# Kernel optimization log

Measured on AMD Instinct MI355X. Metric: run time of the kernel, lower is better.

Reference implementation:

```python
import jax, jax.numpy as jnp
import numpy as np

N, E, C = 25000, 400000, 64
NUM_ELEM, NUM_BESSEL, HID, NPATH, L = 4, 8, 64, 5, 2
R_MAX, AVG_NN = 5.0, 16.0
SQRT3, SQRT2 = 3.0 ** 0.5, 2.0 ** 0.5


def setup_inputs() -> dict:
    key = jax.random.key(0)
    ks = jax.random.split(key, 16)
    def w(k, shape, fan_in):
        return jax.random.normal(k, shape, jnp.float32) / np.float32(np.sqrt(fan_in))
    return {
        "positions": jax.random.normal(ks[0], (N, 3), jnp.float32),
        "species": jax.random.randint(ks[1], (N,), 0, NUM_ELEM, jnp.int32),
        "edge_index": jax.random.randint(ks[2], (2, E), 0, N, jnp.int32),
        "node_embed_W": w(ks[3], (NUM_ELEM, C), NUM_ELEM),
        "lin_up_W0": w(ks[4], (L, C, C), C),
        "lin_up_W1": w(ks[5], (L, C, C), C),
        "mlp_W1": w(ks[6], (L, NUM_BESSEL, HID), NUM_BESSEL),
        "mlp_W2": w(ks[7], (L, HID, HID), HID),
        "mlp_W3": w(ks[8], (L, HID, NPATH * C), HID),
        "lin_W0": w(ks[9], (L, C, C), C),
        "lin_W1": w(ks[10], (L, C, C), C),
        "prod_W0": w(ks[11], (L, NUM_ELEM, 3, C), 3),
        "prod_W1": w(ks[12], (L, NUM_ELEM, 2, C), 2),
        "prod_lin_W0": w(ks[13], (L, C, C), C),
        "prod_lin_W1": w(ks[14], (L, C, C), C),
    }


def _poly_cutoff(r):  # MACE polynomial cutoff, p=6
    p = 6.0
    x = r / R_MAX
    f = (1.0 - 0.5 * (p + 1.0) * (p + 2.0) * x ** 6
         + p * (p + 2.0) * x ** 7 - 0.5 * p * (p + 1.0) * x ** 8)
    return f * (x < 1.0)


def reference(positions, species, edge_index, node_embed_W,
              lin_up_W0, lin_up_W1, mlp_W1, mlp_W2, mlp_W3,
              lin_W0, lin_W1, prod_W0, prod_W1, prod_lin_W0, prod_lin_W1):
    sender, receiver = edge_index[0], edge_index[1]
    vec = positions[sender] - positions[receiver]                  # [E,3]
    r = jnp.maximum(jnp.linalg.norm(vec, axis=-1), 1e-6)           # [E]
    u = vec / r[:, None]
    Y1 = SQRT3 * u                                                 # l=1 SH (component norm); Y0 == 1
    # Bessel radial embedding with polynomial cutoff -> edge_feats [E, NUM_BESSEL]
    n = jnp.arange(1, NUM_BESSEL + 1, dtype=jnp.float32)
    bessel = jnp.sqrt(2.0 / R_MAX) * jnp.sin(n[None, :] * jnp.pi * r[:, None] / R_MAX) / r[:, None]
    edge_feats = bessel * _poly_cutoff(r)[:, None]
    node_attrs = jax.nn.one_hot(species, NUM_ELEM, dtype=jnp.float32)  # [N,4]
    h0 = node_attrs @ node_embed_W                                 # [N,C] scalars
    h1 = jnp.zeros((N, C, 3), jnp.float32)                         # [N,C,3] vectors
    for l in range(L):
        # linear up-projection (per-l channel mixing)
        x0 = h0 @ lin_up_W0[l]
        x1 = jnp.einsum('ncd,ck->nkd', h1, lin_up_W1[l])
        # per-edge radial MLP -> tensor-product path weights [E,5,C]
        tpw = jax.nn.silu(edge_feats @ mlp_W1[l])
        tpw = jax.nn.silu(tpw @ mlp_W2[l])
        tpw = (tpw @ mlp_W3[l]).reshape(E, NPATH, C)
        xs0, xs1 = x0[sender], x1[sender]                          # gather senders
        # CG tensor product (uvu): paths 0x0->0, 0x1->1, 1x0->1, 1x1->0, 1x1->1
        m0 = tpw[:, 0] * xs0 + tpw[:, 3] * (jnp.einsum('ecd,ed->ec', xs1, Y1) / SQRT3)
        m1 = (tpw[:, 1][..., None] * xs0[..., None] * Y1[:, None, :]
              + tpw[:, 2][..., None] * xs1
              + tpw[:, 4][..., None] * jnp.cross(xs1, Y1[:, None, :]) / SQRT2)
        # scatter-sum aggregation over receivers
        M0 = jax.ops.segment_sum(m0, receiver, num_segments=N) / AVG_NN
        M1 = jax.ops.segment_sum(m1, receiver, num_segments=N) / AVG_NN
        h0 = M0 @ lin_W0[l]
        h1 = jnp.einsum('ncd,ck->nkd', M1, lin_W1[l])
        # equivariant product basis (correlation-2 symmetric contraction, element-dependent weights)
        pw0 = jnp.einsum('ne,epc->npc', node_attrs, prod_W0[l])    # [N,3,C]
        paths0 = jnp.stack([h0, h0 * h0, (h1 * h1).sum(-1) / SQRT3], axis=1)
        b0 = (pw0 * paths0).sum(1)
        pw1 = jnp.einsum('ne,epc->npc', node_attrs, prod_W1[l])    # [N,2,C]
        b1 = pw1[:, 0][..., None] * h1 + pw1[:, 1][..., None] * (h0[..., None] * h1)
        h0 = b0 @ prod_lin_W0[l]
        h1 = jnp.einsum('ncd,ck->nkd', b1, prod_lin_W1[l])
    return jnp.concatenate([h0[..., None], h1], axis=-1)           # [N,C,4]
```

## Files before the change

kernel.cpp:

```cpp
#include <hip/hip_runtime.h>
#include <math.h>

#define CDIM 64
#define NBES 8

#define SQRT3_F     1.7320508075688772f
#define INV_SQRT3_F 0.57735026918962576f
#define INV_SQRT2_F 0.70710678118654752f
#define INV_AVG_NN  0.0625f

__device__ __forceinline__ float silu(float x) {
    return x / (1.0f + expf(-x));
}

__global__ __launch_bounds__(256) void k_lin0(
    float* __restrict__ h0, float* __restrict__ h1,
    const int* __restrict__ species, const float* __restrict__ embedW,
    const float* __restrict__ W0, float* __restrict__ x0, int nnodes) {
    const int w = threadIdx.x >> 6, k = threadIdx.x & 63;
    const int n = blockIdx.x * 4 + w;
    if (n >= nnodes) return;
    const float* er = embedW + species[n] * 64;
    float a0 = 0.f;
    for (int c = 0; c < 64; ++c) a0 = fmaf(er[c], W0[c * 64 + k], a0);
    x0[n * 64 + k] = a0;
    h0[n * 64 + k] = 0.f;
    h1[n * 192 + k] = 0.f;
    h1[n * 192 + 64 + k] = 0.f;
    h1[n * 192 + 128 + k] = 0.f;
}

__global__ __launch_bounds__(320, 4) void k_edge0(
    const float* __restrict__ pos, const int* __restrict__ eidx,
    const float* __restrict__ x0,
    const float* __restrict__ W1, const float* __restrict__ W2,
    const float* __restrict__ W3,
    float* __restrict__ M0, float* __restrict__ M1, int nedges) {
    __shared__ __align__(16) float sFEAT[64][8];
    __shared__ float sY1[64][3];
    __shared__ int sSend[64];
    __shared__ int sRecv[64];
    __shared__ __align__(16) float sH2[64 * 68];
    __shared__ __align__(16) float sU0[4352];

    float* const sH1T = sU0;
    float* const sTP = sU0;

    const int t = threadIdx.x;
    const int wv = t >> 6;

    if (t < 64) {
        int e = blockIdx.x * 64 + t;
        int s = 0, r = 0;
        float y0 = 0.f, y1 = 0.f, y2 = 0.f;
        float feats[NBES];
#pragma unroll
        for (int b = 0; b < NBES; ++b) feats[b] = 0.f;
        if (e < nedges) {
            s = eidx[e];
            r = eidx[nedges + e];
            double dx = (double)pos[3 * s + 0] - (double)pos[3 * r + 0];
            double dy = (double)pos[3 * s + 1] - (double)pos[3 * r + 1];
            double dz = (double)pos[3 * s + 2] - (double)pos[3 * r + 2];
            double rr = sqrt(dx * dx + dy * dy + dz * dz);
            if (rr < 1e-6) rr = 1e-6;
            double inv = 1.0 / rr;
            y0 = (float)(1.7320508075688772 * dx * inv);
            y1 = (float)(1.7320508075688772 * dy * inv);
            y2 = (float)(1.7320508075688772 * dz * inv);
            double xx = rr * 0.2;
            double f = 0.0;
            if (xx < 1.0) {
                double x2 = xx * xx, x3 = x2 * xx, x6 = x3 * x3;
                f = 1.0 - 28.0 * x6 + 48.0 * x6 * xx - 21.0 * x6 * x2;
            }
            double pref = 0.63245553203367587 * f * inv;
#pragma unroll
            for (int b = 0; b < NBES; ++b) {
                double arg = (double)(b + 1) * 3.14159265358979324 * rr * 0.2;
                feats[b] = (float)(sin(arg) * pref);
            }
        }
        sSend[t] = s;
        sRecv[t] = r;
        sY1[t][0] = y0; sY1[t][1] = y1; sY1[t][2] = y2;
#pragma unroll
        for (int b = 0; b < NBES; ++b) sFEAT[t][b] = feats[b];
    }
    __syncthreads();

    if (t < 256) {
        const int j = t & 63;
        float w1c[NBES];
#pragma unroll
        for (int b = 0; b < NBES; ++b) w1c[b] = W1[b * 64 + j];
#pragma unroll
        for (int i = 0; i < 16; ++i) {
            int el = wv * 16 + i;
            const float4* fr = (const float4*)(&sFEAT[el][0]);
            float4 f0 = fr[0], f1 = fr[1];
            float acc = 0.f;
            acc = fmaf(f0.x, w1c[0], acc);
            acc = fmaf(f0.y, w1c[1], acc);
            acc = fmaf(f0.z, w1c[2], acc);
            acc = fmaf(f0.w, w1c[3], acc);
            acc = fmaf(f1.x, w1c[4], acc);
            acc = fmaf(f1.y, w1c[5], acc);
            acc = fmaf(f1.z, w1c[6], acc);
            acc = fmaf(f1.w, w1c[7], acc);
            sH1T[j * 68 + el] = silu(acc);
        }
    }
    __syncthreads();

    if (t < 256) {
        const int eg = t >> 4;
        const int j4 = (t & 15) * 4;
        float a00 = 0.f, a01 = 0.f, a02 = 0.f, a03 = 0.f;
        float a10 = 0.f, a11 = 0.f, a12 = 0.f, a13 = 0.f;
        float a20 = 0.f, a21 = 0.f, a22 = 0.f, a23 = 0.f;
        float a30 = 0.f, a31 = 0.f, a32 = 0.f, a33 = 0.f;
#pragma unroll 4
        for (int k = 0; k < 64; ++k) {
            float4 av = *(const float4*)&sH1T[k * 68 + 4 * eg];
            float4 wv4 = *(const float4*)&W2[k * 64 + j4];
            a00 = fmaf(av.x, wv4.x, a00); a01 = fmaf(av.x, wv4.y, a01);
            a02 = fmaf(av.x, wv4.z, a02); a03 = fmaf(av.x, wv4.w, a03);
            a10 = fmaf(av.y, wv4.x, a10); a11 = fmaf(av.y, wv4.y, a11);
            a12 = fmaf(av.y, wv4.z, a12); a13 = fmaf(av.y, wv4.w, a13);
            a20 = fmaf(av.z, wv4.x, a20); a21 = fmaf(av.z, wv4.y, a21);
            a22 = fmaf(av.z, wv4.z, a22); a23 = fmaf(av.z, wv4.w, a23);
            a30 = fmaf(av.w, wv4.x, a30); a31 = fmaf(av.w, wv4.y, a31);
            a32 = fmaf(av.w, wv4.z, a32); a33 = fmaf(av.w, wv4.w, a33);
        }
        *(float4*)&sH2[(4 * eg + 0) * 68 + j4] =
            make_float4(silu(a00), silu(a01), silu(a02), silu(a03));
        *(float4*)&sH2[(4 * eg + 1) * 68 + j4] =
            make_float4(silu(a10), silu(a11), silu(a12), silu(a13));
        *(float4*)&sH2[(4 * eg + 2) * 68 + j4] =
            make_float4(silu(a20), silu(a21), silu(a22), silu(a23));
        *(float4*)&sH2[(4 * eg + 3) * 68 + j4] =
            make_float4(silu(a30), silu(a31), silu(a32), silu(a33));
    }
    __syncthreads();

    const int eb16 = t & 15;
    const int cb8 = (t >> 4) * 8;
    float acc[4][8];
#pragma unroll
    for (int i = 0; i < 4; ++i)
#pragma unroll
        for (int j = 0; j < 8; ++j) acc[i][j] = 0.f;

    if (t < 256) {
#pragma unroll 1
        for (int kt = 0; kt < 16; ++kt) {
            float4 h[4];
#pragma unroll
            for (int i = 0; i < 4; ++i)
                h[i] = *(const float4*)&sH2[(i * 16 + eb16) * 68 + kt * 4];
#pragma unroll
            for (int kk = 0; kk < 4; ++kk) {
                const int k = kt * 4 + kk;
                float4 wa = *(const float4*)&W3[k * 320 + cb8];
                float4 wb = *(const float4*)&W3[k * 320 + cb8 + 4];
#pragma unroll
                for (int i = 0; i < 4; ++i) {
                    float hv = (kk == 0) ? h[i].x
                             : (kk == 1) ? h[i].y
                             : (kk == 2) ? h[i].z
                                         : h[i].w;
                    acc[i][0] = fmaf(hv, wa.x, acc[i][0]);
                    acc[i][1] = fmaf(hv, wa.y, acc[i][1]);
                    acc[i][2] = fmaf(hv, wa.z, acc[i][2]);
                    acc[i][3] = fmaf(hv, wa.w, acc[i][3]);
                    acc[i][4] = fmaf(hv, wb.x, acc[i][4]);
                    acc[i][5] = fmaf(hv, wb.y, acc[i][5]);
                    acc[i][6] = fmaf(hv, wb.z, acc[i][6]);
                    acc[i][7] = fmaf(hv, wb.w, acc[i][7]);
                }
            }
        }
    }

    const int p0 = cb8 >> 6;
    const int c0 = cb8 & 63;
#pragma unroll
    for (int g = 0; g < 4; ++g) {
        if (t < 256) {
            const int row = (p0 * 16 + eb16) * 68 + c0;
            *(float4*)&sTP[row] =
                make_float4(acc[g][0], acc[g][1], acc[g][2], acc[g][3]);
            *(float4*)&sTP[row + 4] =
                make_float4(acc[g][4], acc[g][5], acc[g][6], acc[g][7]);
        }
        __syncthreads();
        for (int v = t; v < 1024; v += 320) {
            int i = v >> 6, cc = v & 63;
            int el = g * 16 + i;
            int s = sSend[el], r = sRecv[el];
            float X0 = x0[s * 64 + cc];
            float Yx = sY1[el][0], Yy = sY1[el][1], Yz = sY1[el][2];
            float t0 = sTP[(0 * 16 + i) * 68 + cc];
            float t1 = sTP[(1 * 16 + i) * 68 + cc];
            float m0 = t0 * X0;
            float m1 = t1 * X0 * INV_AVG_NN;
            atomicAdd(&M0[r * 64 + cc], m0 * INV_AVG_NN);
            atomicAdd(&M1[r * 192 + cc], m1 * Yx);
            atomicAdd(&M1[r * 192 + 64 + cc], m1 * Yy);
            atomicAdd(&M1[r * 192 + 128 + cc], m1 * Yz);
        }
        __syncthreads();
    }
}

__global__ __launch_bounds__(320, 4) void k_edge(
    const float* __restrict__ pos, const int* __restrict__ eidx,
    const float* __restrict__ x0, const float* __restrict__ x1,
    const float* __restrict__ W1, const float* __restrict__ W2,
    const float* __restrict__ W3,
    float* __restrict__ M0, float* __restrict__ M1, int nedges) {
    __shared__ __align__(16) float sFEAT[64][8];
    __shared__ float sY1[64][3];
    __shared__ int sSend[64];
    __shared__ int sRecv[64];
    __shared__ __align__(16) float sH2[64 * 68];
    __shared__ __align__(16) float sU[5440];

    float* const sH1T = sU;
    float* const sTP = sU;

    const int t = threadIdx.x;
    const int eb = t & 7;
    const int cb8 = (t >> 3) * 8;
    const int wv = t >> 6;
    const int c0 = cb8 & 63;

    if (t < 64) {
        int e = blockIdx.x * 64 + t;
        int s = 0, r = 0;
        float y0 = 0.f, y1 = 0.f, y2 = 0.f;
        float feats[NBES];
#pragma unroll
        for (int b = 0; b < NBES; ++b) feats[b] = 0.f;
        if (e < nedges) {
            s = eidx[e];
            r = eidx[nedges + e];
            double dx = (double)pos[3 * s + 0] - (double)pos[3 * r + 0];
            double dy = (double)pos[3 * s + 1] - (double)pos[3 * r + 1];
            double dz = (double)pos[3 * s + 2] - (double)pos[3 * r + 2];
            double rr = sqrt(dx * dx + dy * dy + dz * dz);
            if (rr < 1e-6) rr = 1e-6;
            double inv = 1.0 / rr;
            y0 = (float)(1.7320508075688772 * dx * inv);
            y1 = (float)(1.7320508075688772 * dy * inv);
            y2 = (float)(1.7320508075688772 * dz * inv);
            double xx = rr * 0.2;
            double f = 0.0;
            if (xx < 1.0) {
                double x2 = xx * xx, x3 = x2 * xx, x6 = x3 * x3;
                f = 1.0 - 28.0 * x6 + 48.0 * x6 * xx - 21.0 * x6 * x2;
            }
            double pref = 0.63245553203367587 * f * inv;
#pragma unroll
            for (int b = 0; b < NBES; ++b) {
                double arg = (double)(b + 1) * 3.14159265358979324 * rr * 0.2;
                feats[b] = (float)(sin(arg) * pref);
            }
        }
        sSend[t] = s;
        sRecv[t] = r;
        sY1[t][0] = y0; sY1[t][1] = y1; sY1[t][2] = y2;
#pragma unroll
        for (int b = 0; b < NBES; ++b) sFEAT[t][b] = feats[b];
    }
    __syncthreads();

    if (t < 256) {
        const int j = t & 63;
        float w1c[NBES];
#pragma unroll
        for (int b = 0; b < NBES; ++b) w1c[b] = W1[b * 64 + j];
#pragma unroll
        for (int i = 0; i < 16; ++i) {
            int el = wv * 16 + i;
            const float4* fr = (const float4*)(&sFEAT[el][0]);
            float4 f0 = fr[0], f1 = fr[1];
            float acc = 0.f;
            acc = fmaf(f0.x, w1c[0], acc);
            acc = fmaf(f0.y, w1c[1], acc);
            acc = fmaf(f0.z, w1c[2], acc);
            acc = fmaf(f0.w, w1c[3], acc);
            acc = fmaf(f1.x, w1c[4], acc);
            acc = fmaf(f1.y, w1c[5], acc);
            acc = fmaf(f1.z, w1c[6], acc);
            acc = fmaf(f1.w, w1c[7], acc);
            sH1T[j * 68 + el] = silu(acc);
        }
    }
    __syncthreads();

    if (t < 256) {
        const int eg = t >> 4;
        const int j4 = (t & 15) * 4;
        float a00 = 0.f, a01 = 0.f, a02 = 0.f, a03 = 0.f;
        float a10 = 0.f, a11 = 0.f, a12 = 0.f, a13 = 0.f;
        float a20 = 0.f, a21 = 0.f, a22 = 0.f, a23 = 0.f;
        float a30 = 0.f, a31 = 0.f, a32 = 0.f, a33 = 0.f;
#pragma unroll 4
        for (int k = 0; k < 64; ++k) {
            float4 av = *(const float4*)&sH1T[k * 68 + 4 * eg];
            float4 wv4 = *(const float4*)&W2[k * 64 + j4];
            a00 = fmaf(av.x, wv4.x, a00); a01 = fmaf(av.x, wv4.y, a01);
            a02 = fmaf(av.x, wv4.z, a02); a03 = fmaf(av.x, wv4.w, a03);
            a10 = fmaf(av.y, wv4.x, a10); a11 = fmaf(av.y, wv4.y, a11);
            a12 = fmaf(av.y, wv4.z, a12); a13 = fmaf(av.y, wv4.w, a13);
            a20 = fmaf(av.z, wv4.x, a20); a21 = fmaf(av.z, wv4.y, a21);
            a22 = fmaf(av.z, wv4.z, a22); a23 = fmaf(av.z, wv4.w, a23);
            a30 = fmaf(av.w, wv4.x, a30); a31 = fmaf(av.w, wv4.y, a31);
            a32 = fmaf(av.w, wv4.z, a32); a33 = fmaf(av.w, wv4.w, a33);
        }
        *(float4*)&sH2[(4 * eg + 0) * 68 + j4] =
            make_float4(silu(a00), silu(a01), silu(a02), silu(a03));
        *(float4*)&sH2[(4 * eg + 1) * 68 + j4] =
            make_float4(silu(a10), silu(a11), silu(a12), silu(a13));
        *(float4*)&sH2[(4 * eg + 2) * 68 + j4] =
            make_float4(silu(a20), silu(a21), silu(a22), silu(a23));
        *(float4*)&sH2[(4 * eg + 3) * 68 + j4] =
            make_float4(silu(a30), silu(a31), silu(a32), silu(a33));
    }
    __syncthreads();

    float acc[8][8];
#pragma unroll
    for (int i = 0; i < 8; ++i)
#pragma unroll
        for (int j = 0; j < 8; ++j) acc[i][j] = 0.f;

#pragma unroll 1
    for (int kt = 0; kt < 16; ++kt) {
        float4 h[8];
#pragma unroll
        for (int i = 0; i < 8; ++i)
            h[i] = *(const float4*)&sH2[(i * 8 + eb) * 68 + kt * 4];
#pragma unroll
        for (int kk = 0; kk < 4; ++kk) {
            const int k = kt * 4 + kk;
            float4 wa = *(const float4*)&W3[k * 320 + cb8];
            float4 wb = *(const float4*)&W3[k * 320 + cb8 + 4];
#pragma unroll
            for (int i = 0; i < 8; ++i) {
                float hv = (kk == 0) ? h[i].x
                         : (kk == 1) ? h[i].y
                         : (kk == 2) ? h[i].z
                                     : h[i].w;
                acc[i][0] = fmaf(hv, wa.x, acc[i][0]);
                acc[i][1] = fmaf(hv, wa.y, acc[i][1]);
                acc[i][2] = fmaf(hv, wa.z, acc[i][2]);
                acc[i][3] = fmaf(hv, wa.w, acc[i][3]);
                acc[i][4] = fmaf(hv, wb.x, acc[i][4]);
                acc[i][5] = fmaf(hv, wb.y, acc[i][5]);
                acc[i][6] = fmaf(hv, wb.z, acc[i][6]);
                acc[i][7] = fmaf(hv, wb.w, acc[i][7]);
            }
        }
    }

#pragma unroll
    for (int g = 0; g < 4; ++g) {
        {
            const int rowA = (wv * 16 + eb) * 68 + c0;
            const int rowB = (wv * 16 + 8 + eb) * 68 + c0;
            *(float4*)&sTP[rowA] =
                make_float4(acc[2 * g][0], acc[2 * g][1], acc[2 * g][2], acc[2 * g][3]);
            *(float4*)&sTP[rowA + 4] =
                make_float4(acc[2 * g][4], acc[2 * g][5], acc[2 * g][6], acc[2 * g][7]);
            *(float4*)&sTP[rowB] =
                make_float4(acc[2 * g + 1][0], acc[2 * g + 1][1], acc[2 * g + 1][2], acc[2 * g + 1][3]);
            *(float4*)&sTP[rowB + 4] =
                make_float4(acc[2 * g + 1][4], acc[2 * g + 1][5], acc[2 * g + 1][6], acc[2 * g + 1][7]);
        }
        __syncthreads();
        for (int v = t; v < 1024; v += 320) {
            int i = v >> 6, cc = v & 63;
            int el = g * 16 + i;
            int s = sSend[el], r = sRecv[el];
            float X0 = x0[s * 64 + cc];
            float Xx = x1[s * 192 + cc];
            float Xy = x1[s * 192 + 64 + cc];
            float Xz = x1[s * 192 + 128 + cc];
            float Yx = sY1[el][0], Yy = sY1[el][1], Yz = sY1[el][2];
            float t0 = sTP[(0 * 16 + i) * 68 + cc];
            float t1 = sTP[(1 * 16 + i) * 68 + cc];
            float t2 = sTP[(2 * 16 + i) * 68 + cc];
            float t3 = sTP[(3 * 16 + i) * 68 + cc];
            float t4 = sTP[(4 * 16 + i) * 68 + cc];
            float dotp = Xx * Yx + Xy * Yy + Xz * Yz;
            float m0 = t0 * X0 + t3 * (dotp * INV_SQRT3_F);
            float cx = Xy * Yz - Xz * Yy;
            float cy = Xz * Yx - Xx * Yz;
            float cz = Xx * Yy - Xy * Yx;
            float m1x = t1 * X0 * Yx + t2 * Xx + t4 * (cx * INV_SQRT2_F);
            float m1y = t1 * X0 * Yy + t2 * Xy + t4 * (cy * INV_SQRT2_F);
            float m1z = t1 * X0 * Yz + t2 * Xz + t4 * (cz * INV_SQRT2_F);
            atomicAdd(&M0[r * 64 + cc], m0 * INV_AVG_NN);
            atomicAdd(&M1[r * 192 + cc], m1x * INV_AVG_NN);
            atomicAdd(&M1[r * 192 + 64 + cc], m1y * INV_AVG_NN);
            atomicAdd(&M1[r * 192 + 128 + cc], m1z * INV_AVG_NN);
        }
        __syncthreads();
    }
}

__global__ __launch_bounds__(256) void k_nodelin(
    float* __restrict__ h0, float* __restrict__ h1,
    const int* __restrict__ species,
    const float* __restrict__ linW0, const float* __restrict__ linW1,
    const float* __restrict__ prodW0, const float* __restrict__ prodW1,
    const float* __restrict__ plinW0, const float* __restrict__ plinW1,
    const float* __restrict__ lupW0, const float* __restrict__ lupW1,
    float* __restrict__ x0, float* __restrict__ x1, int nnodes) {
    __shared__ float sh[4][4][64];
    const int w = threadIdx.x >> 6, k = threadIdx.x & 63;
    const int n = blockIdx.x * 4 + w;
    const bool valid = n < nnodes;
    float v0 = valid ? h0[n * 64 + k] : 0.f;
    float v1 = valid ? h1[n * 192 + k] : 0.f;
    float v2 = valid ? h1[n * 192 + 64 + k] : 0.f;
    float v3 = valid ? h1[n * 192 + 128 + k] : 0.f;
    sh[w][0][k] = v0; sh[w][1][k] = v1; sh[w][2][k] = v2; sh[w][3][k] = v3;
    if (valid) {
        h0[n * 64 + k] = 0.f;
        h1[n * 192 + k] = 0.f;
        h1[n * 192 + 64 + k] = 0.f;
        h1[n * 192 + 128 + k] = 0.f;
    }
    __syncthreads();
    float a0 = 0.f, a1 = 0.f, a2 = 0.f, a3 = 0.f;
    for (int c = 0; c < 64; ++c) {
        float w0 = linW0[c * 64 + k], w1 = linW1[c * 64 + k];
        a0 = fmaf(sh[w][0][c], w0, a0);
        a1 = fmaf(sh[w][1][c], w1, a1);
        a2 = fmaf(sh[w][2][c], w1, a2);
        a3 = fmaf(sh[w][3][c], w1, a3);
    }
    int sp = valid ? species[n] : 0;
    float p00 = prodW0[sp * 192 + k];
    float p01 = prodW0[sp * 192 + 64 + k];
    float p02 = prodW0[sp * 192 + 128 + k];
    float p10 = prodW1[sp * 128 + k];
    float p11 = prodW1[sp * 128 + 64 + k];
    float nsq = a1 * a1 + a2 * a2 + a3 * a3;
    float b0 = p00 * a0 + p01 * (a0 * a0) + p02 * (nsq * INV_SQRT3_F);
    float b1x = p10 * a1 + p11 * (a0 * a1);
    float b1y = p10 * a2 + p11 * (a0 * a2);
    float b1z = p10 * a3 + p11 * (a0 * a3);
    __syncthreads();
    sh[w][0][k] = b0; sh[w][1][k] = b1x; sh[w][2][k] = b1y; sh[w][3][k] = b1z;
    __syncthreads();
    a0 = a1 = a2 = a3 = 0.f;
    for (int c = 0; c < 64; ++c) {
        float w0 = plinW0[c * 64 + k], w1 = plinW1[c * 64 + k];
        a0 = fmaf(sh[w][0][c], w0, a0);
        a1 = fmaf(sh[w][1][c], w1, a1);
        a2 = fmaf(sh[w][2][c], w1, a2);
        a3 = fmaf(sh[w][3][c], w1, a3);
    }
    __syncthreads();
    sh[w][0][k] = a0; sh[w][1][k] = a1; sh[w][2][k] = a2; sh[w][3][k] = a3;
    __syncthreads();
    a0 = a1 = a2 = a3 = 0.f;
    for (int c = 0; c < 64; ++c) {
        float w0 = lupW0[c * 64 + k], w1 = lupW1[c * 64 + k];
        a0 = fmaf(sh[w][0][c], w0, a0);
        a1 = fmaf(sh[w][1][c], w1, a1);
        a2 = fmaf(sh[w][2][c], w1, a2);
        a3 = fmaf(sh[w][3][c], w1, a3);
    }
    if (valid) {
        x0[n * 64 + k] = a0;
        x1[n * 192 + k] = a1;
        x1[n * 192 + 64 + k] = a2;
        x1[n * 192 + 128 + k] = a3;
    }
}

__global__ __launch_bounds__(256) void k_nodeout(
    const float* __restrict__ h0, const float* __restrict__ h1,
    const int* __restrict__ species,
    const float* __restrict__ linW0, const float* __restrict__ linW1,
    const float* __restrict__ prodW0, const float* __restrict__ prodW1,
    const float* __restrict__ plinW0, const float* __restrict__ plinW1,
    float4* __restrict__ out, int nnodes) {
    __shared__ float sh[4][4][64];
    const int w = threadIdx.x >> 6, k = threadIdx.x & 63;
    const int n = blockIdx.x * 4 + w;
    const bool valid = n < nnodes;
    float v0 = valid ? h0[n * 64 + k] : 0.f;
    float v1 = valid ? h1[n * 192 + k] : 0.f;
    float v2 = valid ? h1[n * 192 + 64 + k] : 0.f;
    float v3 = valid ? h1[n * 192 + 128 + k] : 0.f;
    sh[w][0][k] = v0; sh[w][1][k] = v1; sh[w][2][k] = v2; sh[w][3][k] = v3;
    __syncthreads();
    float a0 = 0.f, a1 = 0.f, a2 = 0.f, a3 = 0.f;
    for (int c = 0; c < 64; ++c) {
        float w0 = linW0[c * 64 + k], w1 = linW1[c * 64 + k];
        a0 = fmaf(sh[w][0][c], w0, a0);
        a1 = fmaf(sh[w][1][c], w1, a1);
        a2 = fmaf(sh[w][2][c], w1, a2);
        a3 = fmaf(sh[w][3][c], w1, a3);
    }
    int sp = valid ? species[n] : 0;
    float p00 = prodW0[sp * 192 + k];
    float p01 = prodW0[sp * 192 + 64 + k];
    float p02 = prodW0[sp * 192 + 128 + k];
    float p10 = prodW1[sp * 128 + k];
    float p11 = prodW1[sp * 128 + 64 + k];
    float nsq = a1 * a1 + a2 * a2 + a3 * a3;
    float b0 = p00 * a0 + p01 * (a0 * a0) + p02 * (nsq * INV_SQRT3_F);
    float b1x = p10 * a1 + p11 * (a0 * a1);
    float b1y = p10 * a2 + p11 * (a0 * a2);
    float b1z = p10 * a3 + p11 * (a0 * a3);
    __syncthreads();
    sh[w][0][k] = b0; sh[w][1][k] = b1x; sh[w][2][k] = b1y; sh[w][3][k] = b1z;
    __syncthreads();
    a0 = a1 = a2 = a3 = 0.f;
    for (int c = 0; c < 64; ++c) {
        float w0 = plinW0[c * 64 + k], w1 = plinW1[c * 64 + k];
        a0 = fmaf(sh[w][0][c], w0, a0);
        a1 = fmaf(sh[w][1][c], w1, a1);
        a2 = fmaf(sh[w][2][c], w1, a2);
        a3 = fmaf(sh[w][3][c], w1, a3);
    }
    if (valid) out[n * 64 + k] = make_float4(a0, a1, a2, a3);
}

extern "C" void kernel_launch(void* const* d_in, const int* in_sizes, int n_in,
                              void* d_out, int out_size, void* d_ws,
                              size_t ws_size, hipStream_t stream) {
    const float* positions = (const float*)d_in[0];
    const int* species = (const int*)d_in[1];
    const int* eidx = (const int*)d_in[2];
    const float* embedW = (const float*)d_in[3];
    const float* linupW0 = (const float*)d_in[4];
    const float* linupW1 = (const float*)d_in[5];
    const float* mlpW1 = (const float*)d_in[6];
    const float* mlpW2 = (const float*)d_in[7];
    const float* mlpW3 = (const float*)d_in[8];
    const float* linW0 = (const float*)d_in[9];
    const float* linW1 = (const float*)d_in[10];
    const float* prodW0 = (const float*)d_in[11];
    const float* prodW1 = (const float*)d_in[12];
    const float* plinW0 = (const float*)d_in[13];
    const float* plinW1 = (const float*)d_in[14];

    const int nn = in_sizes[0] / 3;
    const int ne = in_sizes[2] / 2;

    float* h0 = (float*)d_ws;
    float* h1 = h0 + (size_t)nn * 64;
    float* x0 = h1 + (size_t)nn * 192;
    float* x1 = x0 + (size_t)nn * 64;

    const int gridNode = (nn + 3) / 4;
    const int gridEdge = (ne + 63) / 64;

    k_lin0<<<gridNode, 256, 0, stream>>>(
        h0, h1, species, embedW, linupW0, x0, nn);
    k_edge0<<<gridEdge, 320, 0, stream>>>(
        positions, eidx, x0, mlpW1, mlpW2, mlpW3, h0, h1, ne);

    k_nodelin<<<gridNode, 256, 0, stream>>>(
        h0, h1, species, linW0, linW1, prodW0, prodW1, plinW0, plinW1,
        linupW0 + 4096, linupW1 + 4096, x0, x1, nn);

    k_edge<<<gridEdge, 320, 0, stream>>>(
        positions, eidx, x0, x1, mlpW1 + 512, mlpW2 + 4096,
        mlpW3 + 20480, h0, h1, ne);

    k_nodeout<<<gridNode, 256, 0, stream>>>(
        h0, h1, species, linW0 + 4096, linW1 + 4096,
        prodW0 + 768, prodW1 + 512, plinW0 + 4096, plinW1 + 4096,
        (float4*)d_out, nn);
}
```

Before: 1.170 ms.

## Sort edges by sender via counting sort before edge kernels

Adds a counting sort (histogram, single-block scan, atomic scatter) that reorders edges by sender index before the two edge kernels. Gathers of positions and per-node features become more local, which should improve cache hit rates on the sender-side loads. Receivers are still scattered, so the atomic scatter-sum is unchanged. The cost is three extra kernels plus a memset each call, including a serial single-block scan, and it only runs when the workspace is large enough.

Measured after the change: 1.253 ms. 7.1% more time.

```diff
diff --git a/kernel.cpp b/kernel.cpp
--- a/kernel.cpp
+++ b/kernel.cpp
@@ -11,6 +11,50 @@
 
 __device__ __forceinline__ float silu(float x) {
     return x / (1.0f + expf(-x));
+}
+
+
+__global__ __launch_bounds__(256) void k_hist(const int* __restrict__ eidx,
+                                              int* __restrict__ cnt, int ne) {
+    int e = blockIdx.x * 256 + threadIdx.x;
+    if (e < ne) atomicAdd(&cnt[eidx[e]], 1);
+}
+
+__global__ __launch_bounds__(1024) void k_scan(int* __restrict__ cnt, int nn) {
+    __shared__ int part[1024];
+    const int t = threadIdx.x;
+    const int chunk = (nn + 1023) / 1024;
+    const int lo = t * chunk;
+    const int hi = min(lo + chunk, nn);
+    int sum = 0;
+    for (int i = lo; i < hi; ++i) sum += cnt[i];
+    part[t] = sum;
+    __syncthreads();
+    for (int off = 1; off < 1024; off <<= 1) {
+        int v = (t >= off) ? part[t - off] : 0;
+        __syncthreads();
+        part[t] += v;
+        __syncthreads();
+    }
+    int run = (t == 0) ? 0 : part[t - 1];
+    for (int i = lo; i < hi; ++i) {
+        int c = cnt[i];
+        cnt[i] = run;
+        run += c;
+    }
+}
+
+__global__ __launch_bounds__(256) void k_scatter(const int* __restrict__ eidx,
+                                                 int* __restrict__ cnt,
+                                                 int* __restrict__ eidx2,
+                                                 int ne) {
+    int e = blockIdx.x * 256 + threadIdx.x;
+    if (e < ne) {
+        int s = eidx[e];
+        int p = atomicAdd(&cnt[s], 1);
+        eidx2[p] = s;
+        eidx2[ne + p] = eidx[ne + e];
+    }
 }
 
 __global__ __launch_bounds__(256) void k_lin0(
@@ -561,21 +605,35 @@
     float* h1 = h0 + (size_t)nn * 64;
     float* x0 = h1 + (size_t)nn * 192;
     float* x1 = x0 + (size_t)nn * 64;
+    int* eidx2 = (int*)(x1 + (size_t)nn * 192);
 
     const int gridNode = (nn + 3) / 4;
     const int gridEdge = (ne + 63) / 64;
+    const int gridE256 = (ne + 255) / 256;
+
+    const size_t needed =
+        ((size_t)nn * 512) * sizeof(float) + (size_t)2 * ne * sizeof(int);
+    const int* eidx_use = eidx;
+    if (ws_size >= needed) {
+        int* cnt = (int*)x1;
+        hipMemsetAsync(cnt, 0, (size_t)nn * sizeof(int), stream);
+        k_hist<<<gridE256, 256, 0, stream>>>(eidx, cnt, ne);
+        k_scan<<<1, 1024, 0, stream>>>(cnt, nn);
+        k_scatter<<<gridE256, 256, 0, stream>>>(eidx, cnt, eidx2, ne);
+        eidx_use = eidx2;
+    }
 
     k_lin0<<<gridNode, 256, 0, stream>>>(
         h0, h1, species, embedW, linupW0, x0, nn);
     k_edge0<<<gridEdge, 320, 0, stream>>>(
-        positions, eidx, x0, mlpW1, mlpW2, mlpW3, h0, h1, ne);
+        positions, eidx_use, x0, mlpW1, mlpW2, mlpW3, h0, h1, ne);
 
     k_nodelin<<<gridNode, 256, 0, stream>>>(
         h0, h1, species, linW0, linW1, prodW0, prodW1, plinW0, plinW1,
         linupW0 + 4096, linupW1 + 4096, x0, x1, nn);
 
     k_edge<<<gridEdge, 320, 0, stream>>>(
-        positions, eidx, x0, x1, mlpW1 + 512, mlpW2 + 4096,
+        positions, eidx_use, x0, x1, mlpW1 + 512, mlpW2 + 4096,
         mlpW3 + 20480, h0, h1, ne);
 
     k_nodeout<<<gridNode, 256, 0, stream>>>(
```
